# Kernel optimization log

Hardware: AMD Instinct MI355X
Metric: run time of the kernel (lower is better)

The kernel has to match this reference:

```python
import jax, jax.numpy as jnp
import numpy as np

NL, B, L, D, V = 8, 8, 2048, 768, 50288
HALT_ID = 50277
EPS = 1e-5


def setup_inputs() -> dict:
    key = jax.random.key(0)
    ks = jax.random.split(key, 6)
    x_steps = jax.random.normal(ks[0], (NL, B, L, D), jnp.float32)
    residual_steps = jax.random.normal(ks[1], (NL, B, L, D), jnp.float32)
    norm_weight = jnp.ones((D,), jnp.float32)
    lm_head_weight = jax.random.normal(ks[2], (V, D), jnp.float32) * 0.02
    ans_starts = jax.random.randint(ks[3], (B,), 1, L)            # valid answer positions
    chain_lens = jax.random.randint(ks[4], (B,), 1, NL + 1)       # ragged chain lengths
    chain_targets = jax.random.randint(ks[5], (B, NL), 0, V)
    # last target of each chain is <HALT> (as in training data)
    chain_targets = chain_targets.at[jnp.arange(B), chain_lens - 1].set(HALT_ID)
    return {
        "x_steps": x_steps,
        "residual_steps": residual_steps,
        "norm_weight": norm_weight,
        "lm_head_weight": lm_head_weight,
        "ans_starts": ans_starts,
        "chain_targets": chain_targets,
        "chain_lens": chain_lens,
    }


def _forward(x_steps, residual_steps, norm_weight, lm_head_weight,
             ans_starts, chain_targets, chain_lens):
    n_loops, Bn, Ln, Dn = x_steps.shape
    Vn = lm_head_weight.shape[0]
    b_idx = jnp.arange(Bn)

    # gather the single answer position per batch (logits_step[b, as_-1, :])
    pos = jnp.clip(ans_starts - 1, 0, Ln - 1)                     # [B]
    xg = x_steps[:, b_idx, pos]                                   # [NL,B,D]
    rg = residual_steps[:, b_idx, pos]                            # [NL,B,D]

    # norm_f(x, residual, prenorm=False) == RMSNorm(x + residual)
    h = xg + rg
    h = h * jax.lax.rsqrt(jnp.mean(h * h, axis=-1, keepdims=True) + EPS) * norm_weight

    # lm_head on the gathered positions only (same math as full logits + gather)
    logits = jnp.einsum("lbd,vd->lbv", h, lm_head_weight)         # [NL,B,V]

    # target id: btgt[min(loop_i, len(btgt)-1)]
    loop_i = jnp.arange(n_loops)[:, None]                         # [NL,1]
    tidx = jnp.minimum(loop_i, chain_lens[None, :] - 1)           # [NL,B]
    tgt = chain_targets[b_idx[None, :], tidx]                     # [NL,B]

    valid = (ans_starts[None, :] >= 1) & (ans_starts[None, :] < Ln) & (tgt < Vn)
    vf = valid.astype(jnp.float32)

    # full-vocab cross entropy per (loop, batch)
    logZ = jax.scipy.special.logsumexp(logits, axis=-1)           # [NL,B]
    tgt_logit = jnp.take_along_axis(logits, tgt[..., None], axis=-1)[..., 0]
    ce = logZ - tgt_logit                                         # [NL,B]

    pred = jnp.argmax(logits, axis=-1)                            # [NL,B]
    correct = (pred == tgt).astype(jnp.float32)

    cnt = vf.sum(axis=1)                                          # valid per loop
    has = cnt > 0
    hasf = has.astype(jnp.float32)
    denom = jnp.maximum(cnt, 1.0)
    loop_loss = jnp.where(has, (ce * vf).sum(axis=1) / denom, 0.0)
    loop_acc = jnp.where(has, (correct * vf).sum(axis=1) / denom, 0.0)

    n_has = hasf.sum()
    avg_loss = (loop_loss * hasf).sum() / jnp.maximum(n_has, 1.0)
    avg_acc = (loop_acc * hasf).sum() / jnp.maximum(n_has, 1.0)

    # answer_acc = mean of step_accs[:-1] (drop last valid loop) if >1 valid loop
    last_valid = n_loops - 1 - jnp.argmax(has[::-1])
    drop_last = hasf * (jnp.arange(n_loops) != last_valid).astype(jnp.float32)
    ans_mask = jnp.where(n_has > 1, drop_last, hasf)
    answer_acc = jnp.where(ans_mask.sum() > 0,
                           (loop_acc * ans_mask).sum() / jnp.maximum(ans_mask.sum(), 1.0),
                           avg_acc)

    hm = vf * (tgt == HALT_ID).astype(jnp.float32)
    halt_acc = jnp.where(hm.sum() > 0,
                         (correct * hm).sum() / jnp.maximum(hm.sum(), 1.0),
                         0.0)
    return avg_loss, avg_acc, answer_acc, halt_acc


def reference(x_steps, residual_steps, norm_weight, lm_head_weight,
              ans_starts, chain_targets, chain_lens):
    return _forward(x_steps, residual_steps, norm_weight, lm_head_weight,
                    ans_starts, chain_targets, chain_lens)
```

## Files before the change

kernel.cpp:

```cpp
#include <hip/hip_runtime.h>
#include <hip/hip_bf16.h>
#include <math.h>

#define NLOOP 8
#define BB 8
#define LLEN 2048
#define DD 768
#define VV 50288
#define HALT 50277
#define EPSF 1e-5f

#define BN 64
#define BKK 32
#define KSTEPS (DD / BKK)
#define NBLK ((VV + BN - 1) / BN)

typedef short bf16x8 __attribute__((ext_vector_type(8)));
typedef float f32x4 __attribute__((ext_vector_type(4)));

__device__ __forceinline__ unsigned short f32_to_bf16(float f) {
    unsigned u = __builtin_bit_cast(unsigned, f);
    unsigned r = (u + 0x7FFFu + ((u >> 16) & 1u)) >> 16;
    return (unsigned short)r;
}

__global__ __launch_bounds__(256) void k_prep(
    const float* __restrict__ x, const float* __restrict__ res,
    const float* __restrict__ nw, const float* __restrict__ W,
    const int* __restrict__ ans_starts, const int* __restrict__ chain_targets,
    const int* __restrict__ chain_lens,
    unsigned short* __restrict__ hbf, float* __restrict__ tgt_logit)
{
    int lb = blockIdx.x, l = lb >> 3, b = lb & 7;
    int tid = threadIdx.x, lane = tid & 63, wave = tid >> 6;
    int as = ans_starts[b];
    int pos = as - 1;
    pos = pos < 0 ? 0 : (pos > LLEN - 1 ? LLEN - 1 : pos);
    size_t base = ((size_t)lb * LLEN + (size_t)pos) * DD;

    float hv[3];
    float ss = 0.f;
#pragma unroll
    for (int i = 0; i < 3; ++i) {
        int d = tid + i * 256;
        float v = x[base + d] + res[base + d];
        hv[i] = v;
        ss += v * v;
    }
#pragma unroll
    for (int off = 32; off; off >>= 1) ss += __shfl_down(ss, off);
    __shared__ float red[4];
    __shared__ float bc;
    if (lane == 0) red[wave] = ss;
    __syncthreads();
    if (tid == 0) bc = red[0] + red[1] + red[2] + red[3];
    __syncthreads();
    float rs = rsqrtf(bc / (float)DD + EPSF);

    int cl = chain_lens[b];
    int tix = l < cl - 1 ? l : cl - 1;
    int tgt = chain_targets[b * NLOOP + tix];
    bool tok = (tgt >= 0) && (tgt < VV);

    float dp = 0.f;
#pragma unroll
    for (int i = 0; i < 3; ++i) {
        int d = tid + i * 256;
        float h = hv[i] * rs * nw[d];
        hbf[(size_t)lb * DD + d] = f32_to_bf16(h);
        if (tok) dp += h * W[(size_t)tgt * DD + d];
    }
#pragma unroll
    for (int off = 32; off; off >>= 1) dp += __shfl_down(dp, off);
    __syncthreads();
    if (lane == 0) red[wave] = dp;
    __syncthreads();
    if (tid == 0) tgt_logit[lb] = red[0] + red[1] + red[2] + red[3];
}

__global__ __launch_bounds__(256) void k_logits(
    const float* __restrict__ W, const unsigned short* __restrict__ hbf,
    float* __restrict__ pmax, float* __restrict__ psum, int* __restrict__ parg)
{
    __shared__ unsigned short As[2][64 * 32];
    __shared__ unsigned short Bs[2][64 * 56];
    __shared__ float wmaxs[4][64];
    __shared__ float wsums[4][64];
    __shared__ int   wargs[4][64];
    __shared__ float bmaxs[64];
    __shared__ int   bargs[64];

    int blk = blockIdx.x;
    int v0 = blk * BN;
    int tid = threadIdx.x;
    int wave = tid >> 6, lane = tid & 63, q = lane >> 4, c = lane & 15;

    int rowa = tid >> 2, sa = tid & 3;
    int kchA = sa ^ ((rowa >> 1) & 3);
    const unsigned short* gA = hbf + (size_t)rowa * DD + kchA * 8;

    int r1 = tid >> 3, koff = (tid & 7) * 4;
    int vB0 = v0 + r1, vB1 = v0 + r1 + 32;
    bool okB0 = vB0 < VV, okB1 = vB1 < VV;
    const float* gB0 = W + (size_t)vB0 * DD + koff;
    const float* gB1 = W + (size_t)vB1 * DD + koff;

    float4 rb0 = make_float4(0.f, 0.f, 0.f, 0.f), rb1 = rb0;

    auto stage = [&](int k0, int bufi) {
        __builtin_amdgcn_global_load_lds(
            (const __attribute__((address_space(1))) unsigned int*)(gA + k0),
            (__attribute__((address_space(3))) unsigned int*)(&As[bufi][wave * 512]),
            16, 0, 0);
        rb0 = okB0 ? *(const float4*)(gB0 + k0) : make_float4(0.f, 0.f, 0.f, 0.f);
        rb1 = okB1 ? *(const float4*)(gB1 + k0) : make_float4(0.f, 0.f, 0.f, 0.f);
    };

    f32x4 acc[4];
#pragma unroll
    for (int m = 0; m < 4; ++m) acc[m] = (f32x4){0.f, 0.f, 0.f, 0.f};

    int slot = q ^ ((c >> 1) & 3);

    stage(0, 0);
    int buf = 0;
    for (int ks = 0; ks < KSTEPS; ++ks) {
        asm volatile("s_waitcnt vmcnt(0)" ::: "memory");
        {
            ushort4 w0, w1;
            w0.x = f32_to_bf16(rb0.x); w0.y = f32_to_bf16(rb0.y);
            w0.z = f32_to_bf16(rb0.z); w0.w = f32_to_bf16(rb0.w);
            w1.x = f32_to_bf16(rb1.x); w1.y = f32_to_bf16(rb1.y);
            w1.z = f32_to_bf16(rb1.z); w1.w = f32_to_bf16(rb1.w);
            *(ushort4*)&Bs[buf][r1 * 56 + koff] = w0;
            *(ushort4*)&Bs[buf][(r1 + 32) * 56 + koff] = w1;
        }
        __syncthreads();
        if (ks + 1 < KSTEPS) stage((ks + 1) * BKK, buf ^ 1);

        bf16x8 bfrag = *(const bf16x8*)&Bs[buf][(wave * 16 + c) * 56 + q * 8];
        bf16x8 a0 = *(const bf16x8*)&As[buf][(c + 0)  * 32 + slot * 8];
        bf16x8 a1 = *(const bf16x8*)&As[buf][(c + 16) * 32 + slot * 8];
        bf16x8 a2 = *(const bf16x8*)&As[buf][(c + 32) * 32 + slot * 8];
        bf16x8 a3 = *(const bf16x8*)&As[buf][(c + 48) * 32 + slot * 8];
        acc[0] = __builtin_amdgcn_mfma_f32_16x16x32_bf16(a0, bfrag, acc[0], 0, 0, 0);
        acc[1] = __builtin_amdgcn_mfma_f32_16x16x32_bf16(a1, bfrag, acc[1], 0, 0, 0);
        acc[2] = __builtin_amdgcn_mfma_f32_16x16x32_bf16(a2, bfrag, acc[2], 0, 0, 0);
        acc[3] = __builtin_amdgcn_mfma_f32_16x16x32_bf16(a3, bfrag, acc[3], 0, 0, 0);
        buf ^= 1;
    }

    int colg = v0 + wave * 16 + c;
    bool cval = colg < VV;
    const float NEGINF = -__builtin_inff();

#pragma unroll
    for (int m = 0; m < 4; ++m) {
#pragma unroll
        for (int r = 0; r < 4; ++r) {
            float val = cval ? acc[m][r] : NEGINF;
            int idx = colg;
#pragma unroll
            for (int off = 1; off < 16; off <<= 1) {
                float ov = __shfl_xor(val, off);
                int oi = __shfl_xor(idx, off);
                if (ov > val || (ov == val && oi < idx)) { val = ov; idx = oi; }
            }
            if (c == 0) {
                int row = 16 * m + 4 * q + r;
                wmaxs[wave][row] = val;
                wargs[wave][row] = idx;
            }
        }
    }
    __syncthreads();
    if (tid < 64) {
        float M = NEGINF; int A_ = 0x7fffffff;
#pragma unroll
        for (int w = 0; w < 4; ++w) {
            float v = wmaxs[w][tid];
            if (v > M) { M = v; A_ = wargs[w][tid]; }
        }
        bmaxs[tid] = M; bargs[tid] = A_;
    }
    __syncthreads();
#pragma unroll
    for (int m = 0; m < 4; ++m) {
#pragma unroll
        for (int r = 0; r < 4; ++r) {
            int row = 16 * m + 4 * q + r;
            float M = bmaxs[row];
            float e = cval ? __expf(acc[m][r] - M) : 0.f;
#pragma unroll
            for (int off = 1; off < 16; off <<= 1) e += __shfl_xor(e, off);
            if (c == 0) wsums[wave][row] = e;
        }
    }
    __syncthreads();
    if (tid < 64) {
        float s = wsums[0][tid] + wsums[1][tid] + wsums[2][tid] + wsums[3][tid];
        pmax[(size_t)tid * NBLK + blk] = bmaxs[tid];
        psum[(size_t)tid * NBLK + blk] = s;
        parg[(size_t)tid * NBLK + blk] = bargs[tid];
    }
}

__global__ __launch_bounds__(256) void k_combine(
    const float* __restrict__ pmax, const float* __restrict__ psum,
    const int* __restrict__ parg, float* __restrict__ logZ, int* __restrict__ pred)
{
    int r = blockIdx.x;
    int tid = threadIdx.x;
    int wave = tid >> 6, lane = tid & 63;
    const float NEGINF = -__builtin_inff();

    const float* pm = pmax + (size_t)r * NBLK;
    const float* ps = psum + (size_t)r * NBLK;
    const int*   pa = parg + (size_t)r * NBLK;

    float M = NEGINF; int A_ = 0x7fffffff;
    for (int i = tid; i < NBLK; i += 256) {
        float m = pm[i];
        int a = pa[i];
        if (m > M || (m == M && a < A_)) { M = m; A_ = a; }
    }
#pragma unroll
    for (int off = 1; off < 64; off <<= 1) {
        float ov = __shfl_xor(M, off);
        int oa = __shfl_xor(A_, off);
        if (ov > M || (ov == M && oa < A_)) { M = ov; A_ = oa; }
    }
    __shared__ float sm[4]; __shared__ int sa[4]; __shared__ float ssum[4];
    if (lane == 0) { sm[wave] = M; sa[wave] = A_; }
    __syncthreads();
    if (tid == 0) {
#pragma unroll
        for (int w = 1; w < 4; ++w)
            if (sm[w] > sm[0] || (sm[w] == sm[0] && sa[w] < sa[0])) { sm[0] = sm[w]; sa[0] = sa[w]; }
    }
    __syncthreads();
    float Mg = sm[0];

    float S = 0.f;
    for (int i = tid; i < NBLK; i += 256)
        S += ps[i] * __expf(pm[i] - Mg);
#pragma unroll
    for (int off = 1; off < 64; off <<= 1) S += __shfl_xor(S, off);
    if (lane == 0) ssum[wave] = S;
    __syncthreads();
    if (tid == 0) {
        logZ[r] = Mg + logf(ssum[0] + ssum[1] + ssum[2] + ssum[3]);
        pred[r] = sa[0];
    }
}

__global__ __launch_bounds__(64) void k_epilogue(
    const float* __restrict__ logZg, const int* __restrict__ predg,
    const float* __restrict__ tgt_logit,
    const int* __restrict__ ans_starts, const int* __restrict__ chain_targets,
    const int* __restrict__ chain_lens, float* __restrict__ out)
{
    __shared__ float logZ[64];
    __shared__ int pred[64];
    int r = threadIdx.x;
    logZ[r] = logZg[r];
    pred[r] = predg[r];
    __syncthreads();
    if (r == 0) {
        float loop_loss[NLOOP], loop_acc[NLOOP], hasf[NLOOP];
        float n_has = 0.f, hms = 0.f, hcs = 0.f;
        for (int l = 0; l < NLOOP; ++l) {
            float cnt = 0.f, se = 0.f, sc = 0.f;
            for (int b = 0; b < BB; ++b) {
                int cl = chain_lens[b];
                int ti = l < cl - 1 ? l : cl - 1;
                int tgt = chain_targets[b * NLOOP + ti];
                int as = ans_starts[b];
                bool valid = (as >= 1) && (as < LLEN) && (tgt < VV);
                int idx = l * BB + b;
                float ce = logZ[idx] - tgt_logit[idx];
                float corr = (pred[idx] == tgt) ? 1.f : 0.f;
                if (valid) {
                    cnt += 1.f; se += ce; sc += corr;
                    if (tgt == HALT) { hms += 1.f; hcs += corr; }
                }
            }
            bool has = cnt > 0.f;
            hasf[l] = has ? 1.f : 0.f;
            n_has += hasf[l];
            float denom = cnt > 1.f ? cnt : 1.f;
            loop_loss[l] = has ? se / denom : 0.f;
            loop_acc[l]  = has ? sc / denom : 0.f;
        }
        float nn = n_has > 1.f ? n_has : 1.f;
        float avg_loss = 0.f, avg_acc = 0.f;
        for (int l = 0; l < NLOOP; ++l) {
            avg_loss += loop_loss[l] * hasf[l];
            avg_acc  += loop_acc[l]  * hasf[l];
        }
        avg_loss /= nn; avg_acc /= nn;
        int last_valid = NLOOP - 1;
        for (int l = NLOOP - 1; l >= 0; --l) if (hasf[l] > 0.f) { last_valid = l; break; }
        float ams = 0.f, aacc = 0.f;
        for (int l = 0; l < NLOOP; ++l) {
            float mask = (n_has > 1.f) ? (hasf[l] * ((l != last_valid) ? 1.f : 0.f)) : hasf[l];
            ams += mask; aacc += loop_acc[l] * mask;
        }
        float answer_acc = (ams > 0.f) ? (aacc / (ams > 1.f ? ams : 1.f)) : avg_acc;
        float halt_acc = (hms > 0.f) ? (hcs / (hms > 1.f ? hms : 1.f)) : 0.f;
        out[0] = avg_loss; out[1] = avg_acc; out[2] = answer_acc; out[3] = halt_acc;
    }
}

extern "C" void kernel_launch(void* const* d_in, const int* in_sizes, int n_in,
                              void* d_out, int out_size, void* d_ws, size_t ws_size,
                              hipStream_t stream) {
    const float* x   = (const float*)d_in[0];
    const float* res = (const float*)d_in[1];
    const float* nw  = (const float*)d_in[2];
    const float* W   = (const float*)d_in[3];
    const int* ans   = (const int*)d_in[4];
    const int* ct    = (const int*)d_in[5];
    const int* cl    = (const int*)d_in[6];
    float* out = (float*)d_out;

    char* ws = (char*)d_ws;
    unsigned short* hbf = (unsigned short*)ws;
    float* tgtl = (float*)(ws + 98304);
    size_t off = 98560;
    float* pmax = (float*)(ws + off);  off += (size_t)64 * NBLK * 4;
    float* psum = (float*)(ws + off);  off += (size_t)64 * NBLK * 4;
    int*   parg = (int*)  (ws + off);  off += (size_t)64 * NBLK * 4;
    float* logZ = (float*)(ws + off);  off += 256;
    int*   pred = (int*)  (ws + off);  off += 256;

    k_prep<<<64, 256, 0, stream>>>(x, res, nw, W, ans, ct, cl, hbf, tgtl);
    k_logits<<<NBLK, 256, 0, stream>>>(W, hbf, pmax, psum, parg);
    k_combine<<<64, 256, 0, stream>>>(pmax, psum, parg, logZ, pred);
    k_epilogue<<<1, 64, 0, stream>>>(logZ, pred, tgtl, ans, ct, cl, out);
}
```

Before: 58.30 us.

## Load GEMM fragments directly to registers and fold epilogue into combine kernel

The logits GEMM no longer stages A and B tiles through LDS with per-step barriers. Each lane loads its bf16 A fragments and fp32 W fragments straight from global memory into registers, double-buffered in registers, with the bf16 conversion done in-register. This removes LDS traffic and __syncthreads from the main loop, but A is now re-read by every wave and the W loads are less coalesced. Separately, the epilogue kernel is merged into k_combine using an atomic counter: the last block to finish computes the final metrics, saving one kernel launch.

```diff
diff --git a/kernel.cpp b/kernel.cpp
--- a/kernel.cpp
+++ b/kernel.cpp
@@ -29,8 +29,11 @@
     const float* __restrict__ nw, const float* __restrict__ W,
     const int* __restrict__ ans_starts, const int* __restrict__ chain_targets,
     const int* __restrict__ chain_lens,
-    unsigned short* __restrict__ hbf, float* __restrict__ tgt_logit)
+    unsigned short* __restrict__ hbf, float* __restrict__ tgt_logit,
+    unsigned int* __restrict__ counter)
 {
+    if (blockIdx.x == 0 && threadIdx.x == 0) *counter = 0u;
+
     int lb = blockIdx.x, l = lb >> 3, b = lb & 7;
     int tid = threadIdx.x, lane = tid & 63, wave = tid >> 6;
     int as = ans_starts[b];
@@ -82,73 +85,70 @@
     const float* __restrict__ W, const unsigned short* __restrict__ hbf,
     float* __restrict__ pmax, float* __restrict__ psum, int* __restrict__ parg)
 {
-    __shared__ unsigned short As[2][64 * 32];
-    __shared__ unsigned short Bs[2][64 * 56];
+    int blk = blockIdx.x;
+    int v0 = blk * BN;
+    int tid = threadIdx.x;
+    int wave = tid >> 6, lane = tid & 63, q = lane >> 4, c = lane & 15;
+
+    int brow = v0 + wave * 16 + c;
+    int browc = brow < VV ? brow : 0;
+    const float* Bp = W + (size_t)browc * DD + q * 8;
+    const unsigned short* Ap = hbf + (size_t)c * DD + q * 8;
+
+    f32x4 acc[4];
+#pragma unroll
+    for (int m = 0; m < 4; ++m) acc[m] = (f32x4){0.f, 0.f, 0.f, 0.f};
+
+    bf16x8 a0_[4]; float4 b0_[2];
+    bf16x8 a1_[4]; float4 b1_[2];
+
+    auto load0 = [&](int ks) {
+        int ko = ks * BKK;
+#pragma unroll
+        for (int m = 0; m < 4; ++m)
+            a0_[m] = *(const bf16x8*)(Ap + (size_t)m * 16 * DD + ko);
+        b0_[0] = *(const float4*)(Bp + ko);
+        b0_[1] = *(const float4*)(Bp + ko + 4);
+    };
+    auto load1 = [&](int ks) {
+        int ko = ks * BKK;
+#pragma unroll
+        for (int m = 0; m < 4; ++m)
+            a1_[m] = *(const bf16x8*)(Ap + (size_t)m * 16 * DD + ko);
+        b1_[0] = *(const float4*)(Bp + ko);
+        b1_[1] = *(const float4*)(Bp + ko + 4);
+    };
+    auto step = [&](bf16x8* a, float4* b) {
+        bf16x8 bf;
+        bf[0] = (short)f32_to_bf16(b[0].x);
+        bf[1] = (short)f32_to_bf16(b[0].y);
+        bf[2] = (short)f32_to_bf16(b[0].z);
+        bf[3] = (short)f32_to_bf16(b[0].w);
+        bf[4] = (short)f32_to_bf16(b[1].x);
+        bf[5] = (short)f32_to_bf16(b[1].y);
+        bf[6] = (short)f32_to_bf16(b[1].z);
+        bf[7] = (short)f32_to_bf16(b[1].w);
+        acc[0] = __builtin_amdgcn_mfma_f32_16x16x32_bf16(a[0], bf, acc[0], 0, 0, 0);
+        acc[1] = __builtin_amdgcn_mfma_f32_16x16x32_bf16(a[1], bf, acc[1], 0, 0, 0);
+        acc[2] = __builtin_amdgcn_mfma_f32_16x16x32_bf16(a[2], bf, acc[2], 0, 0, 0);
+        acc[3] = __builtin_amdgcn_mfma_f32_16x16x32_bf16(a[3], bf, acc[3], 0, 0, 0);
+    };
+
+    load0(0);
+    load1(1);
+#pragma unroll
+    for (int ks = 0; ks < KSTEPS; ks += 2) {
+        step(a0_, b0_);
+        if (ks + 2 < KSTEPS) load0(ks + 2);
+        step(a1_, b1_);
+        if (ks + 3 < KSTEPS) load1(ks + 3);
+    }
+
     __shared__ float wmaxs[4][64];
     __shared__ float wsums[4][64];
     __shared__ int   wargs[4][64];
     __shared__ float bmaxs[64];
     __shared__ int   bargs[64];
-
-    int blk = blockIdx.x;
-    int v0 = blk * BN;
-    int tid = threadIdx.x;
-    int wave = tid >> 6, lane = tid & 63, q = lane >> 4, c = lane & 15;
-
-    int rowa = tid >> 2, sa = tid & 3;
-    int kchA = sa ^ ((rowa >> 1) & 3);
-    const unsigned short* gA = hbf + (size_t)rowa * DD + kchA * 8;
-
-    int r1 = tid >> 3, koff = (tid & 7) * 4;
-    int vB0 = v0 + r1, vB1 = v0 + r1 + 32;
-    bool okB0 = vB0 < VV, okB1 = vB1 < VV;
-    const float* gB0 = W + (size_t)vB0 * DD + koff;
-    const float* gB1 = W + (size_t)vB1 * DD + koff;
-
-    float4 rb0 = make_float4(0.f, 0.f, 0.f, 0.f), rb1 = rb0;
-
-    auto stage = [&](int k0, int bufi) {
-        __builtin_amdgcn_global_load_lds(
-            (const __attribute__((address_space(1))) unsigned int*)(gA + k0),
-            (__attribute__((address_space(3))) unsigned int*)(&As[bufi][wave * 512]),
-            16, 0, 0);
-        rb0 = okB0 ? *(const float4*)(gB0 + k0) : make_float4(0.f, 0.f, 0.f, 0.f);
-        rb1 = okB1 ? *(const float4*)(gB1 + k0) : make_float4(0.f, 0.f, 0.f, 0.f);
-    };
-
-    f32x4 acc[4];
-#pragma unroll
-    for (int m = 0; m < 4; ++m) acc[m] = (f32x4){0.f, 0.f, 0.f, 0.f};
-
-    int slot = q ^ ((c >> 1) & 3);
-
-    stage(0, 0);
-    int buf = 0;
-    for (int ks = 0; ks < KSTEPS; ++ks) {
-        asm volatile("s_waitcnt vmcnt(0)" ::: "memory");
-        {
-            ushort4 w0, w1;
-            w0.x = f32_to_bf16(rb0.x); w0.y = f32_to_bf16(rb0.y);
-            w0.z = f32_to_bf16(rb0.z); w0.w = f32_to_bf16(rb0.w);
-            w1.x = f32_to_bf16(rb1.x); w1.y = f32_to_bf16(rb1.y);
-            w1.z = f32_to_bf16(rb1.z); w1.w = f32_to_bf16(rb1.w);
-            *(ushort4*)&Bs[buf][r1 * 56 + koff] = w0;
-            *(ushort4*)&Bs[buf][(r1 + 32) * 56 + koff] = w1;
-        }
-        __syncthreads();
-        if (ks + 1 < KSTEPS) stage((ks + 1) * BKK, buf ^ 1);
-
-        bf16x8 bfrag = *(const bf16x8*)&Bs[buf][(wave * 16 + c) * 56 + q * 8];
-        bf16x8 a0 = *(const bf16x8*)&As[buf][(c + 0)  * 32 + slot * 8];
-        bf16x8 a1 = *(const bf16x8*)&As[buf][(c + 16) * 32 + slot * 8];
-        bf16x8 a2 = *(const bf16x8*)&As[buf][(c + 32) * 32 + slot * 8];
-        bf16x8 a3 = *(const bf16x8*)&As[buf][(c + 48) * 32 + slot * 8];
-        acc[0] = __builtin_amdgcn_mfma_f32_16x16x32_bf16(a0, bfrag, acc[0], 0, 0, 0);
-        acc[1] = __builtin_amdgcn_mfma_f32_16x16x32_bf16(a1, bfrag, acc[1], 0, 0, 0);
-        acc[2] = __builtin_amdgcn_mfma_f32_16x16x32_bf16(a2, bfrag, acc[2], 0, 0, 0);
-        acc[3] = __builtin_amdgcn_mfma_f32_16x16x32_bf16(a3, bfrag, acc[3], 0, 0, 0);
-        buf ^= 1;
-    }
 
     int colg = v0 + wave * 16 + c;
     bool cval = colg < VV;
@@ -207,7 +207,11 @@
 
 __global__ __launch_bounds__(256) void k_combine(
     const float* __restrict__ pmax, const float* __restrict__ psum,
-    const int* __restrict__ parg, float* __restrict__ logZ, int* __restrict__ pred)
+    const int* __restrict__ parg, const float* __restrict__ tgt_logit,
+    const int* __restrict__ ans_starts, const int* __restrict__ chain_targets,
+    const int* __restrict__ chain_lens,
+    float* __restrict__ logZ, int* __restrict__ pred,
+    unsigned int* __restrict__ counter, float* __restrict__ out)
 {
     int r = blockIdx.x;
     int tid = threadIdx.x;
@@ -231,6 +235,7 @@
         if (ov > M || (ov == M && oa < A_)) { M = ov; A_ = oa; }
     }
     __shared__ float sm[4]; __shared__ int sa[4]; __shared__ float ssum[4];
+    __shared__ int lastflag;
     if (lane == 0) { sm[wave] = M; sa[wave] = A_; }
     __syncthreads();
     if (tid == 0) {
@@ -249,24 +254,24 @@
     if (lane == 0) ssum[wave] = S;
     __syncthreads();
     if (tid == 0) {
-        logZ[r] = Mg + logf(ssum[0] + ssum[1] + ssum[2] + ssum[3]);
-        pred[r] = sa[0];
-    }
-}
-
-__global__ __launch_bounds__(64) void k_epilogue(
-    const float* __restrict__ logZg, const int* __restrict__ predg,
-    const float* __restrict__ tgt_logit,
-    const int* __restrict__ ans_starts, const int* __restrict__ chain_targets,
-    const int* __restrict__ chain_lens, float* __restrict__ out)
-{
-    __shared__ float logZ[64];
-    __shared__ int pred[64];
-    int r = threadIdx.x;
-    logZ[r] = logZg[r];
-    pred[r] = predg[r];
-    __syncthreads();
-    if (r == 0) {
+        float lz = Mg + logf(ssum[0] + ssum[1] + ssum[2] + ssum[3]);
+        __hip_atomic_store(&logZ[r], lz, __ATOMIC_RELAXED, __HIP_MEMORY_SCOPE_AGENT);
+        __hip_atomic_store(&pred[r], sa[0], __ATOMIC_RELAXED, __HIP_MEMORY_SCOPE_AGENT);
+        __threadfence();
+        unsigned int old = atomicAdd(counter, 1u);
+        lastflag = (old == 63u) ? 1 : 0;
+    }
+    __syncthreads();
+    if (lastflag == 0) return;
+
+    __threadfence();
+    __shared__ float lzs[64]; __shared__ int prs[64];
+    if (tid < 64) {
+        lzs[tid] = __hip_atomic_load(&logZ[tid], __ATOMIC_RELAXED, __HIP_MEMORY_SCOPE_AGENT);
+        prs[tid] = __hip_atomic_load(&pred[tid], __ATOMIC_RELAXED, __HIP_MEMORY_SCOPE_AGENT);
+    }
+    __syncthreads();
+    if (tid == 0) {
         float loop_loss[NLOOP], loop_acc[NLOOP], hasf[NLOOP];
         float n_has = 0.f, hms = 0.f, hcs = 0.f;
         for (int l = 0; l < NLOOP; ++l) {
@@ -278,8 +283,8 @@
                 int as = ans_starts[b];
                 bool valid = (as >= 1) && (as < LLEN) && (tgt < VV);
                 int idx = l * BB + b;
-                float ce = logZ[idx] - tgt_logit[idx];
-                float corr = (pred[idx] == tgt) ? 1.f : 0.f;
+                float ce = lzs[idx] - tgt_logit[idx];
+                float corr = (prs[idx] == tgt) ? 1.f : 0.f;
                 if (valid) {
                     cnt += 1.f; se += ce; sc += corr;
                     if (tgt == HALT) { hms += 1.f; hcs += corr; }
@@ -333,9 +338,10 @@
     int*   parg = (int*)  (ws + off);  off += (size_t)64 * NBLK * 4;
     float* logZ = (float*)(ws + off);  off += 256;
     int*   pred = (int*)  (ws + off);  off += 256;
-
-    k_prep<<<64, 256, 0, stream>>>(x, res, nw, W, ans, ct, cl, hbf, tgtl);
+    unsigned int* counter = (unsigned int*)(ws + off); off += 256;
+
+    k_prep<<<64, 256, 0, stream>>>(x, res, nw, W, ans, ct, cl, hbf, tgtl, counter);
     k_logits<<<NBLK, 256, 0, stream>>>(W, hbf, pmax, psum, parg);
-    k_combine<<<64, 256, 0, stream>>>(pmax, psum, parg, logZ, pred);
-    k_epilogue<<<1, 64, 0, stream>>>(logZ, pred, tgtl, ans, ct, cl, out);
-}
+    k_combine<<<64, 256, 0, stream>>>(pmax, psum, parg, tgtl, ans, ct, cl,
+                                      logZ, pred, counter, out);
+}
```

Measured after the change: 100.1 us. 71.7% more time.
